# Kernel optimization log

Hardware: AMD Instinct MI355X
Metric: run time of the kernel (lower is better)

## Reference

```python
import jax, jax.numpy as jnp
import numpy as np

B, T, F, H, HEAD = 8192, 168, 64, 50, 100


def setup_inputs() -> dict:
    key = jax.random.key(0)
    ks = jax.random.split(key, 6)
    scale = lambda k, shape, fan: (jax.random.normal(k, shape, jnp.float32) / np.sqrt(fan)).astype(jnp.float32)
    x = jax.random.normal(ks[0], (B, T, F), jnp.float32)
    Wx = scale(ks[1], (F, 4 * H), F)          # input->gates [i,f,g,o]
    Wh = scale(ks[2], (H, 4 * H), H)          # hidden->gates
    b = jnp.zeros((4 * H,), jnp.float32).at[H:2 * H].set(1.0)  # unit_forget_bias
    W1 = scale(ks[3], (H, HEAD), H)
    b1 = jnp.zeros((HEAD,), jnp.float32)
    W2 = scale(ks[4], (HEAD, 1), HEAD)
    b2 = jnp.zeros((1,), jnp.float32)
    return {"x": x, "Wx": Wx, "Wh": Wh, "b": b, "W1": W1, "b1": b1, "W2": W2, "b2": b2}


def reference(x, Wx, Wh, b, W1, b1, W2, b2):
    # x: [B, T, F]. Unrolled LSTM (Keras LSTMCell: sigmoid gates, tanh activation),
    # take last hidden state, MLP head, residual add of last-step feature 0.
    Bn = x.shape[0]
    Hn = Wh.shape[0]
    h0 = jnp.zeros((Bn, Hn), x.dtype)
    c0 = jnp.zeros((Bn, Hn), x.dtype)

    def step(carry, xt):
        h, c = carry
        z = xt @ Wx + h @ Wh + b           # [B, 4H]
        i, f, g, o = jnp.split(z, 4, axis=-1)
        c = jax.nn.sigmoid(f) * c + jax.nn.sigmoid(i) * jnp.tanh(g)
        h = jax.nn.sigmoid(o) * jnp.tanh(c)
        return (h, c), None

    xs = jnp.swapaxes(x, 0, 1)             # [T, B, F]
    (h_last, _), _ = jax.lax.scan(step, (h0, c0), xs)
    out = jax.nn.relu(h_last @ W1 + b1) @ W2 + b2   # [B, 1]
    return out + x[:, -1, 0:1]
```

## Files before the change

kernel.cpp:

```cpp
#include <hip/hip_runtime.h>


#define B_N 8192
#define T_N 168
#define F_N 64
#define H_N 50
#define HEAD_N 100
#define ROWSTRIDE (T_N * F_N)

typedef _Float16 f16x8 __attribute__((ext_vector_type(8)));
typedef _Float16 f16x4 __attribute__((ext_vector_type(4)));
typedef float    f32x4 __attribute__((ext_vector_type(4)));

#define LOG2E  1.4426950408889634f
#define LOG2E2 2.8853900817779268f

#define MFMA __builtin_amdgcn_mfma_f32_16x16x32_f16

#define BAR()                                                        \
    do {                                                             \
        asm volatile("s_waitcnt lgkmcnt(0)" ::: "memory");           \
        __builtin_amdgcn_s_barrier();                                \
        asm volatile("" ::: "memory");                               \
    } while (0)

__device__ __forceinline__ float rcp_f(float v) { return __builtin_amdgcn_rcpf(v); }
#if __has_builtin(__builtin_amdgcn_exp2f)
__device__ __forceinline__ float exp2_f(float v) { return __builtin_amdgcn_exp2f(v); }
#else
__device__ __forceinline__ float exp2_f(float v) { return __expf(0.6931471805599453f * v); }
#endif

__launch_bounds__(256, 2)
__global__ void lstm_fused(const float* __restrict__ x,
                           const float* __restrict__ Wx,
                           const float* __restrict__ Wh,
                           const float* __restrict__ b,
                           const float* __restrict__ W1,
                           const float* __restrict__ b1,
                           const float* __restrict__ W2,
                           const float* __restrict__ b2,
                           float* __restrict__ out)
{
    __shared__ alignas(16) _Float16 xb[2][16][72];
    __shared__ alignas(16) _Float16 hb[2][16][72];
    __shared__ float hrelu[16][HEAD_N];

    const int tid  = threadIdx.x;
    const int lane = tid & 63;
    const int w    = tid >> 6;
    const int rowA = lane & 15;
    const int kg   = lane >> 4;
    const int R0   = blockIdx.x * 16;

    f16x8 wxf[4][2], whf[4][2];
    float bg[4];
    const int  jl = w * 16 + rowA;
    const bool jv = (jl < H_N);
    #pragma unroll
    for (int g = 0; g < 4; ++g) {
        const float sc = (g == 2) ? LOG2E2 : LOG2E;
        bg[g] = jv ? b[g * H_N + jl] * sc : 0.0f;
        #pragma unroll
        for (int ks = 0; ks < 2; ++ks) {
            f16x8 vx, vh;
            #pragma unroll
            for (int i = 0; i < 8; ++i) {
                int k = ks * 32 + kg * 8 + i;
                float xv = 0.0f, hv = 0.0f;
                if (jv)            xv = Wx[k * 200 + g * H_N + jl] * sc;
                if (jv && k < H_N) hv = Wh[k * 200 + g * H_N + jl] * sc;
                vx[i] = (_Float16)xv;
                vh[i] = (_Float16)hv;
            }
            wxf[g][ks] = vx;
            whf[g][ks] = vh;
        }
    }

    float c0 = 0.f, c1 = 0.f, c2 = 0.f, c3 = 0.f;

    for (int idx = tid; idx < 16 * 72; idx += 256)
        ((_Float16*)hb[0])[idx] = (_Float16)0.0f;

    const int xr  = tid >> 4;
    const int xf0 = (tid & 15) * 4;
    const float* xrow = x + (size_t)(R0 + xr) * ROWSTRIDE + xf0;

    f32x4 xpr0, xpr1;
    {
        f32x4 v0 = *reinterpret_cast<const f32x4*>(xrow);
        f32x4 v1 = *reinterpret_cast<const f32x4*>(xrow + F_N);
        xpr0 = *reinterpret_cast<const f32x4*>(xrow + 2 * F_N);
        xpr1 = *reinterpret_cast<const f32x4*>(xrow + 3 * F_N);
        f16x4 a, c4;
        #pragma unroll
        for (int j = 0; j < 4; ++j) { a[j] = (_Float16)v0[j]; c4[j] = (_Float16)v1[j]; }
        *reinterpret_cast<f16x4*>(&xb[0][xr][xf0]) = a;
        *reinterpret_cast<f16x4*>(&xb[1][xr][xf0]) = c4;
    }
    const float* xld = xrow + 4 * F_N;
    __syncthreads();

    f32x4 axi, axf, axg, axo;
    {
        f16x8 xa0 = *reinterpret_cast<const f16x8*>(&xb[0][rowA][kg * 8]);
        f16x8 xa1 = *reinterpret_cast<const f16x8*>(&xb[0][rowA][32 + kg * 8]);
        axi = (f32x4){bg[0], bg[0], bg[0], bg[0]};
        axf = (f32x4){bg[1], bg[1], bg[1], bg[1]};
        axg = (f32x4){bg[2], bg[2], bg[2], bg[2]};
        axo = (f32x4){bg[3], bg[3], bg[3], bg[3]};
        axi = MFMA(xa0, wxf[0][0], axi, 0, 0, 0);
        axf = MFMA(xa0, wxf[1][0], axf, 0, 0, 0);
        axg = MFMA(xa0, wxf[2][0], axg, 0, 0, 0);
        axo = MFMA(xa0, wxf[3][0], axo, 0, 0, 0);
        axi = MFMA(xa1, wxf[0][1], axi, 0, 0, 0);
        axf = MFMA(xa1, wxf[1][1], axf, 0, 0, 0);
        axg = MFMA(xa1, wxf[2][1], axg, 0, 0, 0);
        axo = MFMA(xa1, wxf[3][1], axo, 0, 0, 0);
    }
    __syncthreads();

#define GATE1(PW, ii, cvar)                                                    \
    {                                                                          \
        float si_ = rcp_f(1.0f + exp2_f(-zi[ii]));                             \
        float sf_ = rcp_f(1.0f + exp2_f(-zf[ii]));                             \
        float tg_ = fmaf(-2.0f, rcp_f(1.0f + exp2_f(zg[ii])), 1.0f);           \
        float so_ = rcp_f(1.0f + exp2_f(-zo[ii]));                             \
        float cn_ = fmaf(sf_, cvar, si_ * tg_);                                \
        cvar = cn_;                                                            \
        float tc_ = fmaf(-2.0f, rcp_f(1.0f + exp2_f(LOG2E2 * cn_)), 1.0f);     \
        hb[PW][kg * 4 + ii][jl] = (_Float16)(so_ * tc_);                       \
    }

#define STEP(P, DO_XF, DO_XW, DO_LOAD)                                         \
    {                                                                          \
        f16x8 ha0 = *reinterpret_cast<const f16x8*>(&hb[P][rowA][kg * 8]);     \
        f16x8 ha1 = *reinterpret_cast<const f16x8*>(&hb[P][rowA][32 + kg * 8]);\
        f32x4 zi = MFMA(ha0, whf[0][0], axi, 0, 0, 0);                         \
        f32x4 zf = MFMA(ha0, whf[1][0], axf, 0, 0, 0);                         \
        f32x4 zg = MFMA(ha0, whf[2][0], axg, 0, 0, 0);                         \
        f32x4 zo = MFMA(ha0, whf[3][0], axo, 0, 0, 0);                         \
        zi = MFMA(ha1, whf[0][1], zi, 0, 0, 0);                                \
        zf = MFMA(ha1, whf[1][1], zf, 0, 0, 0);                                \
        zg = MFMA(ha1, whf[2][1], zg, 0, 0, 0);                                \
        zo = MFMA(ha1, whf[3][1], zo, 0, 0, 0);                                \
        if (DO_XF) {               \
            f16x8 xa0 = *reinterpret_cast<const f16x8*>(&xb[P ^ 1][rowA][kg * 8]);      \
            f16x8 xa1 = *reinterpret_cast<const f16x8*>(&xb[P ^ 1][rowA][32 + kg * 8]); \
            axi = (f32x4){bg[0], bg[0], bg[0], bg[0]};                         \
            axf = (f32x4){bg[1], bg[1], bg[1], bg[1]};                         \
            axg = (f32x4){bg[2], bg[2], bg[2], bg[2]};                         \
            axo = (f32x4){bg[3], bg[3], bg[3], bg[3]};                         \
            axi = MFMA(xa0, wxf[0][0], axi, 0, 0, 0);                          \
            axf = MFMA(xa0, wxf[1][0], axf, 0, 0, 0);                          \
            axg = MFMA(xa0, wxf[2][0], axg, 0, 0, 0);                          \
            axo = MFMA(xa0, wxf[3][0], axo, 0, 0, 0);                          \
            axi = MFMA(xa1, wxf[0][1], axi, 0, 0, 0);                          \
            axf = MFMA(xa1, wxf[1][1], axf, 0, 0, 0);                          \
            axg = MFMA(xa1, wxf[2][1], axg, 0, 0, 0);                          \
            axo = MFMA(xa1, wxf[3][1], axo, 0, 0, 0);                          \
        }                                                                      \
        if (DO_XW) {     \
            f16x4 xc;                                                          \
            xc[0] = (_Float16)xpr##P[0]; xc[1] = (_Float16)xpr##P[1];          \
            xc[2] = (_Float16)xpr##P[2]; xc[3] = (_Float16)xpr##P[3];          \
            *reinterpret_cast<f16x4*>(&xb[P][xr][xf0]) = xc;                   \
        }                                                                      \
        if (DO_LOAD) { xpr##P = *reinterpret_cast<const f32x4*>(xld); xld += F_N; } \
        GATE1(P ^ 1, 0, c0)                                                    \
        GATE1(P ^ 1, 1, c1)                                                    \
        GATE1(P ^ 1, 2, c2)                                                    \
        GATE1(P ^ 1, 3, c3)                                                    \
        BAR();                                                                 \
    }

    for (int it = 0; it < 82; ++it) {
        STEP(0, 1, 1, 1)
        STEP(1, 1, 1, 1)
    }
    STEP(0, 1, 1, 0)
    STEP(1, 1, 1, 0)
    STEP(0, 1, 0, 0)
    STEP(1, 0, 0, 0)
#undef STEP
#undef GATE1

    {
        const int r1 = tid & 15;
        const int u1 = tid >> 4;
        float hrow[H_N];
        #pragma unroll
        for (int k = 0; k < H_N; ++k) hrow[k] = (float)hb[0][r1][k];
        for (int uu = u1; uu < HEAD_N; uu += 16) {
            float s = b1[uu];
            #pragma unroll
            for (int k = 0; k < H_N; ++k) s += hrow[k] * W1[k * HEAD_N + uu];
            hrelu[r1][uu] = fmaxf(s, 0.0f);
        }
    }
    __syncthreads();
    {
        const int r2 = tid >> 4;
        const int p  = tid & 15;
        float s = 0.0f;
        for (int uu = p; uu < HEAD_N; uu += 16) s += hrelu[r2][uu] * W2[uu];
        #pragma unroll
        for (int off = 8; off > 0; off >>= 1) s += __shfl_xor(s, off, 16);
        if (p == 0) {
            float res = x[(size_t)(R0 + r2) * ROWSTRIDE + (T_N - 1) * F_N + 0];
            out[R0 + r2] = s + b2[0] + res;
        }
    }
}

extern "C" void kernel_launch(void* const* d_in, const int* in_sizes, int n_in,
                              void* d_out, int out_size, void* d_ws, size_t ws_size,
                              hipStream_t stream) {
    const float* x  = (const float*)d_in[0];
    const float* Wx = (const float*)d_in[1];
    const float* Wh = (const float*)d_in[2];
    const float* b  = (const float*)d_in[3];
    const float* W1 = (const float*)d_in[4];
    const float* b1 = (const float*)d_in[5];
    const float* W2 = (const float*)d_in[6];
    const float* b2 = (const float*)d_in[7];
    float* out = (float*)d_out;

    lstm_fused<<<dim3(B_N / 16), dim3(256), 0, stream>>>(x, Wx, Wh, b, W1, b1, W2, b2, out);
}
```

Measured before the change: 165.6 us.

## Split input projection and recurrence into producer/consumer warp groups

Doubles the block to 512 threads. Four waves now compute the input projection x@Wx one step ahead and stage it in a shared-memory double buffer. The other four waves run the hidden recurrence and gates at raised priority, reading the staged projections. This takes the input-projection MFMAs off the serial recurrence critical path, at the cost of extra LDS traffic, more shared memory, and larger blocks that may lower occupancy.

```diff
diff --git a/kernel.cpp b/kernel.cpp
--- a/kernel.cpp
+++ b/kernel.cpp
@@ -31,7 +31,7 @@
 __device__ __forceinline__ float exp2_f(float v) { return __expf(0.6931471805599453f * v); }
 #endif
 
-__launch_bounds__(256, 2)
+__launch_bounds__(512, 4)
 __global__ void lstm_fused(const float* __restrict__ x,
                            const float* __restrict__ Wx,
                            const float* __restrict__ Wh,
@@ -44,51 +44,64 @@
 {
     __shared__ alignas(16) _Float16 xb[2][16][72];
     __shared__ alignas(16) _Float16 hb[2][16][72];
+    __shared__ alignas(16) float axb[2][4][4][64][4];
     __shared__ float hrelu[16][HEAD_N];
 
     const int tid  = threadIdx.x;
     const int lane = tid & 63;
     const int w    = tid >> 6;
+    const int ut   = w & 3;
     const int rowA = lane & 15;
     const int kg   = lane >> 4;
     const int R0   = blockIdx.x * 16;
+    const int jl   = ut * 16 + rowA;
+    const bool jv  = (jl < H_N);
 
     f16x8 wxf[4][2], whf[4][2];
     float bg[4];
-    const int  jl = w * 16 + rowA;
-    const bool jv = (jl < H_N);
-    #pragma unroll
-    for (int g = 0; g < 4; ++g) {
-        const float sc = (g == 2) ? LOG2E2 : LOG2E;
-        bg[g] = jv ? b[g * H_N + jl] * sc : 0.0f;
-        #pragma unroll
-        for (int ks = 0; ks < 2; ++ks) {
-            f16x8 vx, vh;
+    if (w < 4) {
+        #pragma unroll
+        for (int g = 0; g < 4; ++g) {
+            const float sc = (g == 2) ? LOG2E2 : LOG2E;
+            bg[g] = jv ? b[g * H_N + jl] * sc : 0.0f;
             #pragma unroll
-            for (int i = 0; i < 8; ++i) {
-                int k = ks * 32 + kg * 8 + i;
-                float xv = 0.0f, hv = 0.0f;
-                if (jv)            xv = Wx[k * 200 + g * H_N + jl] * sc;
-                if (jv && k < H_N) hv = Wh[k * 200 + g * H_N + jl] * sc;
-                vx[i] = (_Float16)xv;
-                vh[i] = (_Float16)hv;
+            for (int ks = 0; ks < 2; ++ks) {
+                f16x8 v;
+                #pragma unroll
+                for (int i = 0; i < 8; ++i) {
+                    int k = ks * 32 + kg * 8 + i;
+                    v[i] = (_Float16)(jv ? Wx[k * 200 + g * H_N + jl] * sc : 0.0f);
+                }
+                wxf[g][ks] = v;
             }
-            wxf[g][ks] = vx;
-            whf[g][ks] = vh;
+        }
+    } else {
+        #pragma unroll
+        for (int g = 0; g < 4; ++g) {
+            const float sc = (g == 2) ? LOG2E2 : LOG2E;
+            #pragma unroll
+            for (int ks = 0; ks < 2; ++ks) {
+                f16x8 v;
+                #pragma unroll
+                for (int i = 0; i < 8; ++i) {
+                    int k = ks * 32 + kg * 8 + i;
+                    v[i] = (_Float16)((jv && k < H_N) ? Wh[k * 200 + g * H_N + jl] * sc : 0.0f);
+                }
+                whf[g][ks] = v;
+            }
         }
     }
 
     float c0 = 0.f, c1 = 0.f, c2 = 0.f, c3 = 0.f;
 
-    for (int idx = tid; idx < 16 * 72; idx += 256)
+    for (int idx = tid; idx < 16 * 72; idx += 512)
         ((_Float16*)hb[0])[idx] = (_Float16)0.0f;
 
-    const int xr  = tid >> 4;
+    const int xr  = (tid >> 4) & 15;
     const int xf0 = (tid & 15) * 4;
     const float* xrow = x + (size_t)(R0 + xr) * ROWSTRIDE + xf0;
-
     f32x4 xpr0, xpr1;
-    {
+    if (w < 4) {
         f32x4 v0 = *reinterpret_cast<const f32x4*>(xrow);
         f32x4 v1 = *reinterpret_cast<const f32x4*>(xrow + F_N);
         xpr0 = *reinterpret_cast<const f32x4*>(xrow + 2 * F_N);
@@ -102,22 +115,25 @@
     const float* xld = xrow + 4 * F_N;
     __syncthreads();
 
-    f32x4 axi, axf, axg, axo;
-    {
+    if (w < 4) {
         f16x8 xa0 = *reinterpret_cast<const f16x8*>(&xb[0][rowA][kg * 8]);
         f16x8 xa1 = *reinterpret_cast<const f16x8*>(&xb[0][rowA][32 + kg * 8]);
-        axi = (f32x4){bg[0], bg[0], bg[0], bg[0]};
-        axf = (f32x4){bg[1], bg[1], bg[1], bg[1]};
-        axg = (f32x4){bg[2], bg[2], bg[2], bg[2]};
-        axo = (f32x4){bg[3], bg[3], bg[3], bg[3]};
-        axi = MFMA(xa0, wxf[0][0], axi, 0, 0, 0);
-        axf = MFMA(xa0, wxf[1][0], axf, 0, 0, 0);
-        axg = MFMA(xa0, wxf[2][0], axg, 0, 0, 0);
-        axo = MFMA(xa0, wxf[3][0], axo, 0, 0, 0);
-        axi = MFMA(xa1, wxf[0][1], axi, 0, 0, 0);
-        axf = MFMA(xa1, wxf[1][1], axf, 0, 0, 0);
-        axg = MFMA(xa1, wxf[2][1], axg, 0, 0, 0);
-        axo = MFMA(xa1, wxf[3][1], axo, 0, 0, 0);
+        f32x4 a0 = {bg[0], bg[0], bg[0], bg[0]};
+        f32x4 a1 = {bg[1], bg[1], bg[1], bg[1]};
+        f32x4 a2 = {bg[2], bg[2], bg[2], bg[2]};
+        f32x4 a3 = {bg[3], bg[3], bg[3], bg[3]};
+        a0 = MFMA(xa0, wxf[0][0], a0, 0, 0, 0);
+        a1 = MFMA(xa0, wxf[1][0], a1, 0, 0, 0);
+        a2 = MFMA(xa0, wxf[2][0], a2, 0, 0, 0);
+        a3 = MFMA(xa0, wxf[3][0], a3, 0, 0, 0);
+        a0 = MFMA(xa1, wxf[0][1], a0, 0, 0, 0);
+        a1 = MFMA(xa1, wxf[1][1], a1, 0, 0, 0);
+        a2 = MFMA(xa1, wxf[2][1], a2, 0, 0, 0);
+        a3 = MFMA(xa1, wxf[3][1], a3, 0, 0, 0);
+        *reinterpret_cast<f32x4*>(&axb[0][ut][0][lane][0]) = a0;
+        *reinterpret_cast<f32x4*>(&axb[0][ut][1][lane][0]) = a1;
+        *reinterpret_cast<f32x4*>(&axb[0][ut][2][lane][0]) = a2;
+        *reinterpret_cast<f32x4*>(&axb[0][ut][3][lane][0]) = a3;
     }
     __syncthreads();
 
@@ -133,60 +149,85 @@
         hb[PW][kg * 4 + ii][jl] = (_Float16)(so_ * tc_);                       \
     }
 
-#define STEP(P, DO_XF, DO_XW, DO_LOAD)                                         \
+#define XSTEP(P, DO_XW, DO_LOAD)                                               \
     {                                                                          \
-        f16x8 ha0 = *reinterpret_cast<const f16x8*>(&hb[P][rowA][kg * 8]);     \
-        f16x8 ha1 = *reinterpret_cast<const f16x8*>(&hb[P][rowA][32 + kg * 8]);\
-        f32x4 zi = MFMA(ha0, whf[0][0], axi, 0, 0, 0);                         \
-        f32x4 zf = MFMA(ha0, whf[1][0], axf, 0, 0, 0);                         \
-        f32x4 zg = MFMA(ha0, whf[2][0], axg, 0, 0, 0);                         \
-        f32x4 zo = MFMA(ha0, whf[3][0], axo, 0, 0, 0);                         \
-        zi = MFMA(ha1, whf[0][1], zi, 0, 0, 0);                                \
-        zf = MFMA(ha1, whf[1][1], zf, 0, 0, 0);                                \
-        zg = MFMA(ha1, whf[2][1], zg, 0, 0, 0);                                \
-        zo = MFMA(ha1, whf[3][1], zo, 0, 0, 0);                                \
-        if (DO_XF) {               \
-            f16x8 xa0 = *reinterpret_cast<const f16x8*>(&xb[P ^ 1][rowA][kg * 8]);      \
-            f16x8 xa1 = *reinterpret_cast<const f16x8*>(&xb[P ^ 1][rowA][32 + kg * 8]); \
-            axi = (f32x4){bg[0], bg[0], bg[0], bg[0]};                         \
-            axf = (f32x4){bg[1], bg[1], bg[1], bg[1]};                         \
-            axg = (f32x4){bg[2], bg[2], bg[2], bg[2]};                         \
-            axo = (f32x4){bg[3], bg[3], bg[3], bg[3]};                         \
-            axi = MFMA(xa0, wxf[0][0], axi, 0, 0, 0);                          \
-            axf = MFMA(xa0, wxf[1][0], axf, 0, 0, 0);                          \
-            axg = MFMA(xa0, wxf[2][0], axg, 0, 0, 0);                          \
-            axo = MFMA(xa0, wxf[3][0], axo, 0, 0, 0);                          \
-            axi = MFMA(xa1, wxf[0][1], axi, 0, 0, 0);                          \
-            axf = MFMA(xa1, wxf[1][1], axf, 0, 0, 0);                          \
-            axg = MFMA(xa1, wxf[2][1], axg, 0, 0, 0);                          \
-            axo = MFMA(xa1, wxf[3][1], axo, 0, 0, 0);                          \
-        }                                                                      \
-        if (DO_XW) {     \
+        f16x8 xa0 = *reinterpret_cast<const f16x8*>(&xb[P ^ 1][rowA][kg * 8]);      \
+        f16x8 xa1 = *reinterpret_cast<const f16x8*>(&xb[P ^ 1][rowA][32 + kg * 8]); \
+        f32x4 a0 = {bg[0], bg[0], bg[0], bg[0]};                               \
+        f32x4 a1 = {bg[1], bg[1], bg[1], bg[1]};                               \
+        f32x4 a2 = {bg[2], bg[2], bg[2], bg[2]};                               \
+        f32x4 a3 = {bg[3], bg[3], bg[3], bg[3]};                               \
+        a0 = MFMA(xa0, wxf[0][0], a0, 0, 0, 0);                                \
+        a1 = MFMA(xa0, wxf[1][0], a1, 0, 0, 0);                                \
+        a2 = MFMA(xa0, wxf[2][0], a2, 0, 0, 0);                                \
+        a3 = MFMA(xa0, wxf[3][0], a3, 0, 0, 0);                                \
+        a0 = MFMA(xa1, wxf[0][1], a0, 0, 0, 0);                                \
+        a1 = MFMA(xa1, wxf[1][1], a1, 0, 0, 0);                                \
+        a2 = MFMA(xa1, wxf[2][1], a2, 0, 0, 0);                                \
+        a3 = MFMA(xa1, wxf[3][1], a3, 0, 0, 0);                                \
+        *reinterpret_cast<f32x4*>(&axb[P ^ 1][ut][0][lane][0]) = a0;           \
+        *reinterpret_cast<f32x4*>(&axb[P ^ 1][ut][1][lane][0]) = a1;           \
+        *reinterpret_cast<f32x4*>(&axb[P ^ 1][ut][2][lane][0]) = a2;           \
+        *reinterpret_cast<f32x4*>(&axb[P ^ 1][ut][3][lane][0]) = a3;           \
+        if (DO_XW) {                                                           \
             f16x4 xc;                                                          \
             xc[0] = (_Float16)xpr##P[0]; xc[1] = (_Float16)xpr##P[1];          \
             xc[2] = (_Float16)xpr##P[2]; xc[3] = (_Float16)xpr##P[3];          \
             *reinterpret_cast<f16x4*>(&xb[P][xr][xf0]) = xc;                   \
         }                                                                      \
         if (DO_LOAD) { xpr##P = *reinterpret_cast<const f32x4*>(xld); xld += F_N; } \
+        BAR();                                                                 \
+    }
+
+#define HSTEP(P)                                                               \
+    {                                                                          \
+        __builtin_amdgcn_s_setprio(1);                                         \
+        f16x8 ha0 = *reinterpret_cast<const f16x8*>(&hb[P][rowA][kg * 8]);     \
+        f16x8 ha1 = *reinterpret_cast<const f16x8*>(&hb[P][rowA][32 + kg * 8]);\
+        f32x4 zi = *reinterpret_cast<const f32x4*>(&axb[P][ut][0][lane][0]);   \
+        f32x4 zf = *reinterpret_cast<const f32x4*>(&axb[P][ut][1][lane][0]);   \
+        f32x4 zg = *reinterpret_cast<const f32x4*>(&axb[P][ut][2][lane][0]);   \
+        f32x4 zo = *reinterpret_cast<const f32x4*>(&axb[P][ut][3][lane][0]);   \
+        zi = MFMA(ha0, whf[0][0], zi, 0, 0, 0);                                \
+        zf = MFMA(ha0, whf[1][0], zf, 0, 0, 0);                                \
+        zg = MFMA(ha0, whf[2][0], zg, 0, 0, 0);                                \
+        zo = MFMA(ha0, whf[3][0], zo, 0, 0, 0);                                \
+        zi = MFMA(ha1, whf[0][1], zi, 0, 0, 0);                                \
+        zf = MFMA(ha1, whf[1][1], zf, 0, 0, 0);                                \
+        zg = MFMA(ha1, whf[2][1], zg, 0, 0, 0);                                \
+        zo = MFMA(ha1, whf[3][1], zo, 0, 0, 0);                                \
         GATE1(P ^ 1, 0, c0)                                                    \
         GATE1(P ^ 1, 1, c1)                                                    \
         GATE1(P ^ 1, 2, c2)                                                    \
         GATE1(P ^ 1, 3, c3)                                                    \
+        __builtin_amdgcn_s_setprio(0);                                         \
         BAR();                                                                 \
     }
 
-    for (int it = 0; it < 82; ++it) {
-        STEP(0, 1, 1, 1)
-        STEP(1, 1, 1, 1)
-    }
-    STEP(0, 1, 1, 0)
-    STEP(1, 1, 1, 0)
-    STEP(0, 1, 0, 0)
-    STEP(1, 0, 0, 0)
-#undef STEP
+    if (w < 4) {
+        for (int it = 0; it < 82; ++it) {
+            XSTEP(0, 1, 1)
+            XSTEP(1, 1, 1)
+        }
+        XSTEP(0, 1, 0)
+        XSTEP(1, 1, 0)
+        XSTEP(0, 0, 0)
+        BAR();
+    } else {
+        for (int it = 0; it < 82; ++it) {
+            HSTEP(0)
+            HSTEP(1)
+        }
+        HSTEP(0)
+        HSTEP(1)
+        HSTEP(0)
+        HSTEP(1)
+    }
+#undef XSTEP
+#undef HSTEP
 #undef GATE1
 
-    {
+    if (tid < 256) {
         const int r1 = tid & 15;
         const int u1 = tid >> 4;
         float hrow[H_N];
@@ -200,7 +241,7 @@
         }
     }
     __syncthreads();
-    {
+    if (tid < 256) {
         const int r2 = tid >> 4;
         const int p  = tid & 15;
         float s = 0.0f;
@@ -227,5 +268,5 @@
     const float* b2 = (const float*)d_in[7];
     float* out = (float*)d_out;
 
-    lstm_fused<<<dim3(B_N / 16), dim3(256), 0, stream>>>(x, Wx, Wh, b, W1, b1, W2, b2, out);
+    lstm_fused<<<dim3(B_N / 16), dim3(512), 0, stream>>>(x, Wx, Wh, b, W1, b1, W2, b2, out);
 }
```

Result: faster. 151.8 us (-8.4%).
